# Kernel tuning notes

Measured on AMD Instinct MI355X. Metric: run time of the kernel, lower is better.

Reference implementation:

```python
import jax, jax.numpy as jnp
import numpy as np

WS = 7
NUM_HEADS = 4


def _rel_pos_index(ws):
    # Swin-style relative position index for a ws x ws window -> (ws*ws, ws*ws)
    coords = np.stack(np.meshgrid(np.arange(ws), np.arange(ws), indexing='ij'))
    flat = coords.reshape(2, -1)
    rel = (flat[:, :, None] - flat[:, None, :]).transpose(1, 2, 0)
    rel = rel + (ws - 1)
    return jnp.asarray(rel[..., 0] * (2 * ws - 1) + rel[..., 1])


def setup_inputs() -> dict:
    key = jax.random.key(0)
    ks = jax.random.split(key, 8)
    B, H, W, C = 8, 224, 224, 128
    r = C // 8  # channel-attention reduction
    s = 0.02
    return {
        'x': jax.random.normal(ks[0], (B, H * W, C), jnp.float32),
        'H': H,
        'W': W,
        'ca_w1': jax.random.normal(ks[1], (r, C), jnp.float32) * s,
        'ca_b1': jnp.zeros((r,), jnp.float32),
        'ca_w2': jax.random.normal(ks[2], (C, r), jnp.float32) * s,
        'ca_b2': jnp.zeros((C,), jnp.float32),
        'sa_w': jax.random.normal(ks[3], (1, 2, 7, 7), jnp.float32) * s,
        'sa_b': jnp.zeros((1,), jnp.float32),
        'in_proj_w': jax.random.normal(ks[4], (3 * C, C), jnp.float32) * s,
        'in_proj_b': jnp.zeros((3 * C,), jnp.float32),
        'out_proj_w': jax.random.normal(ks[5], (C, C), jnp.float32) * s,
        'out_proj_b': jnp.zeros((C,), jnp.float32),
        'rpe_table': jax.random.normal(ks[6], ((2 * WS - 1) ** 2, NUM_HEADS), jnp.float32) * s,
    }


def reference(x, H, W, ca_w1, ca_b1, ca_w2, ca_b2, sa_w, sa_b,
              in_proj_w, in_proj_b, out_proj_w, out_proj_b, rpe_table):
    B, N, C = x.shape
    x = x.reshape(B, H, W, C)

    # --- ComprehensiveAttentionalBlock (channel + spatial attention) on NCHW ---
    x4 = x.transpose(0, 3, 1, 2)  # (B, C, H, W)
    pooled = x4.mean(axis=(2, 3))  # (B, C)
    s_ca = jax.nn.sigmoid(jax.nn.relu(pooled @ ca_w1.T + ca_b1) @ ca_w2.T + ca_b2)
    x4 = x4 * s_ca[:, :, None, None]
    sa_in = jnp.concatenate([x4.mean(axis=1, keepdims=True), x4.max(axis=1, keepdims=True)], axis=1)
    sa = jax.lax.conv_general_dilated(sa_in, sa_w, (1, 1), [(3, 3), (3, 3)],
                                      dimension_numbers=('NCHW', 'OIHW', 'NCHW'))
    sa = sa + sa_b[None, :, None, None]
    x4 = x4 * jax.nn.sigmoid(sa)
    x = x4.transpose(0, 2, 3, 1)  # (B, H, W, C)

    # --- pad to multiple of window size (symmetric, as PadBlock) ---
    ph, pw = (-H) % WS, (-W) % WS
    x = jnp.pad(x, ((0, 0), (ph // 2, ph - ph // 2), (pw // 2, pw - pw // 2), (0, 0)))
    Hp, Wp = H + ph, W + pw
    nh, nw = Hp // WS, Wp // WS
    L = WS * WS
    Nb = B * nh * nw

    # --- interlaced window permute: (B,Hp,Wp,C) -> (L, Nb, C) ---
    xp = x.reshape(B, nh, WS, nw, WS, C).transpose(2, 4, 0, 1, 3, 5).reshape(L, Nb, C)

    # --- multi-head attention with relative position embedding ---
    qkv = xp @ in_proj_w.T + in_proj_b  # (L, Nb, 3C)
    q, k, v = jnp.split(qkv, 3, axis=-1)
    d = C // NUM_HEADS
    q = q.reshape(L, Nb, NUM_HEADS, d) * (d ** -0.5)
    k = k.reshape(L, Nb, NUM_HEADS, d)
    v = v.reshape(L, Nb, NUM_HEADS, d)
    scores = jnp.einsum('lnhd,mnhd->nhlm', q, k)  # (Nb, h, L, L)
    bias = rpe_table[_rel_pos_index(WS)]  # (L, L, h)
    scores = scores + bias.transpose(2, 0, 1)[None]
    attn = jax.nn.softmax(scores, axis=-1)
    out = jnp.einsum('nhlm,mnhd->lnhd', attn, v).reshape(L, Nb, C)
    out = out @ out_proj_w.T + out_proj_b

    # --- reverse permute and depad ---
    out = out.reshape(WS, WS, B, nh, nw, C).transpose(2, 3, 0, 4, 1, 5).reshape(B, Hp, Wp, C)
    out = out[:, ph // 2:ph // 2 + H, pw // 2:pw // 2 + W, :]
    return out.reshape(B, N, C)
```

## Files before the change

kernel.cpp:

```cpp
#include <hip/hip_runtime.h>

typedef unsigned short u16;
typedef __attribute__((ext_vector_type(8))) short short8;
typedef __attribute__((ext_vector_type(4))) float f32x4;
typedef __attribute__((ext_vector_type(4))) unsigned short us4;
typedef __attribute__((ext_vector_type(2))) unsigned int u32x2;

union S8U { short8 v; us4 h[2]; unsigned int u[4]; };

__device__ __forceinline__ u16 f2bf(float f){
  unsigned int u = __builtin_bit_cast(unsigned int, f);
  u += 0x7fffu + ((u >> 16) & 1u);
  return (u16)(u >> 16);
}
__device__ __forceinline__ float bf2f(u16 s){
  unsigned int u = ((unsigned int)s) << 16;
  return __builtin_bit_cast(float, u);
}
__device__ __forceinline__ unsigned int cvt2(float a, float b){
  unsigned int r;
  asm("v_cvt_pk_bf16_f32 %0, %1, %2" : "=v"(r) : "v"(a), "v"(b));
  return r;
}
#define MFMA16(a,b,c) __builtin_amdgcn_mfma_f32_16x16x32_bf16((a),(b),(c),0,0,0)

__global__ void k0_prep(const float* __restrict__ w_in, const float* __restrict__ w_out,
                        const float* __restrict__ rpe,
                        u16* __restrict__ wqkv_bf, u16* __restrict__ wout_bf,
                        u16* __restrict__ bias_bf, float* __restrict__ pooled){
  int gid = blockIdx.x * 256 + threadIdx.x;
  int stride = gridDim.x * 256;
  for (int idx = gid; idx < 83968; idx += stride) {
    if (idx < 49152) {
      wqkv_bf[idx] = f2bf(w_in[idx]);
    } else if (idx < 65536) {
      int i = idx - 49152; wout_bf[i] = f2bf(w_out[i]);
    } else if (idx < 81920) {
      int i = idx - 65536;
      int h = i >> 12, l = (i >> 6) & 63, m = i & 63;
      float v;
      if (m >= 49) v = -3.0e38f;
      else if (l >= 49) v = 0.0f;
      else {
        int il = (l * 9363) >> 16, jl = l - il * 7;
        int im = (m * 9363) >> 16, jm = m - im * 7;
        int r = (il - im + 6) * 13 + (jl - jm + 6);
        v = rpe[r * 4 + h];
      }
      bias_bf[i] = f2bf(v);
    } else {
      pooled[idx - 81920] = 0.0f;
    }
  }
}

__global__ void k1_pool(const float* __restrict__ x, float* __restrict__ pooled){
  __shared__ float4 red[4][32];
  int b = blockIdx.x / 392, s = blockIdx.x % 392;
  int t = threadIdx.x;
  int c4 = t & 31, r0 = t >> 5;
  const float4* xb = (const float4*)x + ((size_t)b * 50176 + (size_t)s * 128) * 32;
  float4 acc = {0.f, 0.f, 0.f, 0.f};
#pragma unroll
  for (int i = 0; i < 16; ++i) {
    float4 v = xb[(size_t)(r0 + 8 * i) * 32 + c4];
    acc.x += v.x; acc.y += v.y; acc.z += v.z; acc.w += v.w;
  }
  acc.x += __shfl_xor(acc.x, 32); acc.y += __shfl_xor(acc.y, 32);
  acc.z += __shfl_xor(acc.z, 32); acc.w += __shfl_xor(acc.w, 32);
  if ((t & 63) < 32) red[t >> 6][c4] = acc;
  __syncthreads();
  if (t < 32) {
    float4 a0 = red[0][t], a1 = red[1][t], a2 = red[2][t], a3 = red[3][t];
    float sx = a0.x + a1.x + a2.x + a3.x;
    float sy = a0.y + a1.y + a2.y + a3.y;
    float sz = a0.z + a1.z + a2.z + a3.z;
    float sw = a0.w + a1.w + a2.w + a3.w;
    float* p = pooled + b * 128 + t * 4;
    atomicAdd(p + 0, sx); atomicAdd(p + 1, sy);
    atomicAdd(p + 2, sz); atomicAdd(p + 3, sw);
  }
}

__global__ void k2_mlp(const float* __restrict__ pooled,
                       const float* __restrict__ w1, const float* __restrict__ b1,
                       const float* __restrict__ w2, const float* __restrict__ b2,
                       float* __restrict__ sca){
  __shared__ float hid[8][16];
  int t = threadIdx.x;
  int b = t >> 4, j = t & 15;
  float a = 0.f;
  for (int c = 0; c < 128; ++c) a += pooled[b * 128 + c] * w1[j * 128 + c];
  a = a * (1.0f / 50176.0f) + b1[j];
  hid[b][j] = fmaxf(a, 0.0f);
  __syncthreads();
  int c = t;
  for (int bb = 0; bb < 8; ++bb) {
    float v = b2[c];
    for (int jj = 0; jj < 16; ++jj) v += hid[bb][jj] * w2[c * 16 + jj];
    sca[bb * 128 + c] = 1.0f / (1.0f + __expf(-v));
  }
}

__global__ void k3_stats(const float* __restrict__ x, const float* __restrict__ sca,
                         float* __restrict__ smean, float* __restrict__ smax){
  int b = blockIdx.x / 1568, chunk = blockIdx.x % 1568;
  int t = threadIdx.x, lane = t & 63, wv = t >> 6;
  int p = lane >> 3, c8 = lane & 7;
  const float4* sc = (const float4*)(sca + b * 128 + c8 * 16);
  float4 s0 = sc[0], s1 = sc[1], s2 = sc[2], s3 = sc[3];
  int pix = chunk * 32 + wv * 8 + p;
  const float4* row = (const float4*)(x + ((size_t)b * 50176 + pix) * 128 + c8 * 16);
  float4 v0 = row[0], v1 = row[1], v2 = row[2], v3 = row[3];
  float sum = 0.f, mx = -3.0e38f;
#define ACC4(V,S) { float a0=V.x*S.x, a1=V.y*S.y, a2=V.z*S.z, a3=V.w*S.w; \
                    sum += a0+a1+a2+a3; mx = fmaxf(mx, fmaxf(fmaxf(a0,a1), fmaxf(a2,a3))); }
  ACC4(v0,s0) ACC4(v1,s1) ACC4(v2,s2) ACC4(v3,s3)
#undef ACC4
  sum += __shfl_xor(sum, 1); sum += __shfl_xor(sum, 2); sum += __shfl_xor(sum, 4);
  mx = fmaxf(mx, __shfl_xor(mx, 1));
  mx = fmaxf(mx, __shfl_xor(mx, 2));
  mx = fmaxf(mx, __shfl_xor(mx, 4));
  if (c8 == 0) {
    smean[(size_t)b * 50176 + pix] = sum * (1.0f / 128.0f);
    smax [(size_t)b * 50176 + pix] = mx;
  }
}

__global__ void k4_conv(const float* __restrict__ smean, const float* __restrict__ smax,
                        const float* __restrict__ w, const float* __restrict__ sb,
                        float* __restrict__ ssa){
  __shared__ float tM[22 * 22], tX[22 * 22], wl[98];
  int b = blockIdx.x / 196, cell = blockIdx.x % 196;
  int y0 = (cell / 14) * 16, x0 = (cell % 14) * 16;
  int t = threadIdx.x;
  if (t < 98) wl[t] = w[t];
  for (int idx = t; idx < 484; idx += 256) {
    int yy = y0 - 3 + idx / 22, xx = x0 - 3 + idx % 22;
    bool ok = (yy >= 0 && yy < 224 && xx >= 0 && xx < 224);
    tM[idx] = ok ? smean[(size_t)b * 50176 + yy * 224 + xx] : 0.0f;
    tX[idx] = ok ? smax [(size_t)b * 50176 + yy * 224 + xx] : 0.0f;
  }
  __syncthreads();
  int ty = t >> 4, tx = t & 15;
  float acc = sb[0];
  for (int ky = 0; ky < 7; ++ky)
    for (int kx = 0; kx < 7; ++kx) {
      acc += wl[ky * 7 + kx]      * tM[(ty + ky) * 22 + tx + kx];
      acc += wl[49 + ky * 7 + kx] * tX[(ty + ky) * 22 + tx + kx];
    }
  ssa[(size_t)b * 50176 + (y0 + ty) * 224 + (x0 + tx)] = 1.0f / (1.0f + __expf(-acc));
}

__global__ __launch_bounds__(256) void k5_attn(
    const float* __restrict__ x, const float* __restrict__ sca, const float* __restrict__ ssa,
    const u16* __restrict__ wqkv, const u16* __restrict__ wout, const u16* __restrict__ biasb,
    const float* __restrict__ bin, const float* __restrict__ bout, float* __restrict__ out)
{
  __shared__ u16 lds[26112];
  u16* qR = lds;
  u16* kR = lds + 8704;
  u16* vR = lds + 17408;
  float* fbuf = (float*)(lds + 8704);

  int blk = blockIdx.x;
  int b = blk >> 10, ih = (blk >> 5) & 31, iw = blk & 31;
  int t = threadIdx.x, lane = t & 63, wv = t >> 6;
  int c15 = lane & 15, g4 = lane >> 4;

  {
    int cq = t & 31, rr = t >> 5;
    const float* xb = x + (size_t)b * 50176 * 128;
    float4 s4 = *(const float4*)(sca + b * 128 + cq * 4);
    for (int p = 0; p < 7; ++p) {
      int r = p * 8 + rr;
      if (r < 49) {
        int i = (r * 9363) >> 16, j = r - i * 7;
        int hh = ih * 7 + i, ww = iw * 7 + j;
        float4 v = *(const float4*)(xb + ((size_t)(hh * 224 + ww)) * 128 + cq * 4);
        float ss = ssa[(size_t)b * 50176 + hh * 224 + ww];
        u32x2 o;
        o[0] = cvt2(v.x * s4.x * ss, v.y * s4.y * ss);
        o[1] = cvt2(v.z * s4.z * ss, v.w * s4.w * ss);
        *(u32x2*)(qR + r * 136 + cq * 4) = o;
      }
    }
    unsigned int* z = (unsigned int*)(qR + 49 * 136);
    for (int idx = t; idx < 1020; idx += 256) z[idx] = 0u;
  }
  __syncthreads();

  short8 xsf[4][4];
#pragma unroll
  for (int nt = 0; nt < 4; ++nt)
#pragma unroll
    for (int ks = 0; ks < 4; ++ks)
      xsf[nt][ks] = *(const short8*)(qR + (16 * nt + c15) * 136 + 32 * ks + 8 * g4);
  __syncthreads();

#pragma unroll
  for (int qi = 0; qi < 4; ++qi) {
    int mt = (qi < 2) ? (2 * wv + qi) : (8 + 2 * wv + qi - 2);
    short8 wf[4];
#pragma unroll
    for (int ks = 0; ks < 4; ++ks)
      wf[ks] = *(const short8*)(wqkv + (size_t)(16 * mt + c15) * 128 + 32 * ks + 8 * g4);
    float4 b4 = *(const float4*)(bin + 16 * mt + 4 * g4);
    bool isq = (qi < 2);
    float scl = isq ? 0.17677669529663689f : 1.0f;
    u16* dst = isq ? qR : kR;
    int dcol = isq ? (16 * mt) : (16 * (mt - 8));
#pragma unroll
    for (int nt = 0; nt < 4; ++nt) {
      f32x4 acc = {0.f, 0.f, 0.f, 0.f};
#pragma unroll
      for (int ks = 0; ks < 4; ++ks) acc = MFMA16(wf[ks], xsf[nt][ks], acc);
      u32x2 o;
      o[0] = cvt2((acc[0] + b4.x) * scl, (acc[1] + b4.y) * scl);
      o[1] = cvt2((acc[2] + b4.z) * scl, (acc[3] + b4.w) * scl);
      *(u32x2*)(dst + (16 * nt + c15) * 136 + dcol + 4 * g4) = o;
    }
  }
#pragma unroll
  for (int vi = 0; vi < 2; ++vi) {
    int ntv = 2 * wv + vi;
    short8 wf[4];
#pragma unroll
    for (int ks = 0; ks < 4; ++ks)
      wf[ks] = *(const short8*)(wqkv + (size_t)(256 + 16 * ntv + c15) * 128 + 32 * ks + 8 * g4);
    float bv = bin[256 + 16 * ntv + c15];
#pragma unroll
    for (int mt = 0; mt < 4; ++mt) {
      f32x4 acc = {0.f, 0.f, 0.f, 0.f};
#pragma unroll
      for (int ks = 0; ks < 4; ++ks) acc = MFMA16(xsf[mt][ks], wf[ks], acc);
      u32x2 o;
      o[0] = cvt2(acc[0] + bv, acc[1] + bv);
      o[1] = cvt2(acc[2] + bv, acc[3] + bv);
      *(u32x2*)(vR + (16 * ntv + c15) * 68 + 16 * mt + 4 * g4) = o;
    }
  }

  short8 kf[4], qf[4];
#pragma unroll
  for (int mt = 0; mt < 4; ++mt)
    kf[mt] = *(const short8*)(kR + (16 * mt + c15) * 136 + 32 * wv + 8 * g4);
#pragma unroll
  for (int nt = 0; nt < 4; ++nt)
    qf[nt] = *(const short8*)(qR + (16 * nt + c15) * 136 + 32 * wv + 8 * g4);
  f32x4 sc[4][4];
#pragma unroll
  for (int mt = 0; mt < 4; ++mt)
#pragma unroll
    for (int nt = 0; nt < 4; ++nt) {
      f32x4 zz = {0.f, 0.f, 0.f, 0.f};
      sc[mt][nt] = MFMA16(kf[mt], qf[nt], zz);
    }
#pragma unroll
  for (int mt = 0; mt < 4; ++mt)
#pragma unroll
    for (int nt = 0; nt < 4; ++nt) {
      us4 bb = *(const us4*)(biasb + (size_t)((wv * 64 + 16 * nt + c15) * 64 + 16 * mt + 4 * g4));
      sc[mt][nt][0] += bf2f(bb[0]); sc[mt][nt][1] += bf2f(bb[1]);
      sc[mt][nt][2] += bf2f(bb[2]); sc[mt][nt][3] += bf2f(bb[3]);
    }
  unsigned int pk[4][4][2];
#pragma unroll
  for (int nt = 0; nt < 4; ++nt) {
    float m = -3.0e38f;
#pragma unroll
    for (int mt = 0; mt < 4; ++mt)
      m = fmaxf(m, fmaxf(fmaxf(sc[mt][nt][0], sc[mt][nt][1]),
                         fmaxf(sc[mt][nt][2], sc[mt][nt][3])));
    m = fmaxf(m, __shfl_xor(m, 16));
    m = fmaxf(m, __shfl_xor(m, 32));
    float s = 0.f;
#pragma unroll
    for (int mt = 0; mt < 4; ++mt)
#pragma unroll
      for (int r = 0; r < 4; ++r) {
        float e = __expf(sc[mt][nt][r] - m);
        sc[mt][nt][r] = e; s += e;
      }
    s += __shfl_xor(s, 16);
    s += __shfl_xor(s, 32);
    float rs = 1.0f / s;
#pragma unroll
    for (int mt = 0; mt < 4; ++mt) {
      pk[mt][nt][0] = cvt2(sc[mt][nt][0] * rs, sc[mt][nt][1] * rs);
      pk[mt][nt][1] = cvt2(sc[mt][nt][2] * rs, sc[mt][nt][3] * rs);
    }
  }

  f32x4 oacc[2][4];
  const f32x4 zero4 = {0.f, 0.f, 0.f, 0.f};
#pragma unroll
  for (int dt = 0; dt < 2; ++dt)
#pragma unroll
    for (int nt = 0; nt < 4; ++nt) oacc[dt][nt] = zero4;
#pragma unroll
  for (int ks = 0; ks < 2; ++ks) {
    short8 va[2];
#pragma unroll
    for (int dt = 0; dt < 2; ++dt) {
      S8U u;
      u.h[0] = *(const us4*)(vR + (32 * wv + 16 * dt + c15) * 68 + 32 * ks + 4 * g4);
      u.h[1] = *(const us4*)(vR + (32 * wv + 16 * dt + c15) * 68 + 32 * ks + 16 + 4 * g4);
      va[dt] = u.v;
    }
#pragma unroll
    for (int nt = 0; nt < 4; ++nt) {
      S8U pb;
      pb.u[0] = pk[2 * ks][nt][0];     pb.u[1] = pk[2 * ks][nt][1];
      pb.u[2] = pk[2 * ks + 1][nt][0]; pb.u[3] = pk[2 * ks + 1][nt][1];
#pragma unroll
      for (int dt = 0; dt < 2; ++dt)
        oacc[dt][nt] = MFMA16(va[dt], pb.v, oacc[dt][nt]);
    }
  }
#pragma unroll
  for (int dt = 0; dt < 2; ++dt)
#pragma unroll
    for (int nt = 0; nt < 4; ++nt) {
      u32x2 o;
      o[0] = cvt2(oacc[dt][nt][0], oacc[dt][nt][1]);
      o[1] = cvt2(oacc[dt][nt][2], oacc[dt][nt][3]);
      *(u32x2*)(qR + (16 * nt + c15) * 136 + 32 * wv + 16 * dt + 4 * g4) = o;
    }
  __syncthreads();

  short8 oof[4][4];
#pragma unroll
  for (int mt = 0; mt < 4; ++mt)
#pragma unroll
    for (int ks = 0; ks < 4; ++ks)
      oof[mt][ks] = *(const short8*)(qR + (16 * mt + c15) * 136 + 32 * ks + 8 * g4);
#pragma unroll
  for (int oi = 0; oi < 2; ++oi) {
    int nto = 2 * wv + oi;
    short8 wf[4];
#pragma unroll
    for (int ks = 0; ks < 4; ++ks)
      wf[ks] = *(const short8*)(wout + (size_t)(16 * nto + c15) * 128 + 32 * ks + 8 * g4);
    float bo = bout[16 * nto + c15];
#pragma unroll
    for (int mt = 0; mt < 4; ++mt) {
      f32x4 acc = {0.f, 0.f, 0.f, 0.f};
#pragma unroll
      for (int ks = 0; ks < 4; ++ks) acc = MFMA16(oof[mt][ks], wf[ks], acc);
#pragma unroll
      for (int r = 0; r < 4; ++r)
        fbuf[(16 * mt + 4 * g4 + r) * 132 + 16 * nto + c15] = acc[r] + bo;
    }
  }
  __syncthreads();

  {
    float* ob = out + (size_t)b * 50176 * 128;
    int rr = t >> 5, c = t & 31;
#pragma unroll
    for (int it = 0; it < 7; ++it) {
      int tok = it * 8 + rr;
      if (tok < 49) {
        int i = (tok * 9363) >> 16, j = tok - i * 7;
        int hh = ih * 7 + i, ww = iw * 7 + j;
        float4 vv = *(const float4*)(fbuf + tok * 132 + c * 4);
        *(float4*)(ob + ((size_t)(hh * 224 + ww)) * 128 + c * 4) = vv;
      }
    }
  }
}

extern "C" void kernel_launch(void* const* d_in, const int* in_sizes, int n_in,
                              void* d_out, int out_size, void* d_ws, size_t ws_size,
                              hipStream_t stream) {
  const float* x     = (const float*)d_in[0];
  const float* ca_w1 = (const float*)d_in[3];
  const float* ca_b1 = (const float*)d_in[4];
  const float* ca_w2 = (const float*)d_in[5];
  const float* ca_b2 = (const float*)d_in[6];
  const float* sa_w  = (const float*)d_in[7];
  const float* sa_b  = (const float*)d_in[8];
  const float* w_in  = (const float*)d_in[9];
  const float* b_in  = (const float*)d_in[10];
  const float* w_out = (const float*)d_in[11];
  const float* b_out = (const float*)d_in[12];
  const float* rpe   = (const float*)d_in[13];
  float* out = (float*)d_out;

  char* ws = (char*)d_ws;
  float* pooled = (float*)(ws + 0);
  float* sca    = (float*)(ws + 4096);
  float* smean  = (float*)(ws + 8192);
  float* smax   = (float*)(ws + 8192 + 1605632);
  float* ssa    = (float*)(ws + 8192 + 2 * 1605632);
  u16* wqkv_bf  = (u16*)(ws + 8192 + 3 * 1605632);
  u16* wout_bf  = (u16*)(ws + 8192 + 3 * 1605632 + 98304);
  u16* bias_bf  = (u16*)(ws + 8192 + 3 * 1605632 + 98304 + 32768);

  k0_prep<<<328, 256, 0, stream>>>(w_in, w_out, rpe, wqkv_bf, wout_bf, bias_bf, pooled);
  k1_pool<<<3136, 256, 0, stream>>>(x, pooled);
  k2_mlp <<<1, 128, 0, stream>>>(pooled, ca_w1, ca_b1, ca_w2, ca_b2, sca);
  k3_stats<<<12544, 256, 0, stream>>>(x, sca, smean, smax);
  k4_conv<<<1568, 256, 0, stream>>>(smean, smax, sa_w, sa_b, ssa);
  k5_attn<<<8192, 256, 0, stream>>>(x, sca, ssa, wqkv_bf, wout_bf, bias_bf, b_in, b_out, out);
}
```

Baseline: 659.7 us.

## Shrink attention LDS by aliasing K and V buffers; fold fp32 bias into MFMA accumulator

The attention kernel's shared memory drops from three bf16 tiles to two. K fragments are read into registers before the V tile overwrites the same region, and the output staging buffer reuses the Q region after an extra barrier. The relative-position bias is now stored as fp32 and loaded directly as the MFMA accumulator init, which removes the separate bf16 unpack-and-add pass. The intent is higher occupancy from lower LDS use, paid for with extra __syncthreads and a larger bias table read.

Measured after the change: 671.2 us. Within noise of the previous version (+1.7%).

```diff
diff --git a/kernel.cpp b/kernel.cpp
--- a/kernel.cpp
+++ b/kernel.cpp
@@ -13,10 +13,6 @@
   u += 0x7fffu + ((u >> 16) & 1u);
   return (u16)(u >> 16);
 }
-__device__ __forceinline__ float bf2f(u16 s){
-  unsigned int u = ((unsigned int)s) << 16;
-  return __builtin_bit_cast(float, u);
-}
 __device__ __forceinline__ unsigned int cvt2(float a, float b){
   unsigned int r;
   asm("v_cvt_pk_bf16_f32 %0, %1, %2" : "=v"(r) : "v"(a), "v"(b));
@@ -27,7 +23,7 @@
 __global__ void k0_prep(const float* __restrict__ w_in, const float* __restrict__ w_out,
                         const float* __restrict__ rpe,
                         u16* __restrict__ wqkv_bf, u16* __restrict__ wout_bf,
-                        u16* __restrict__ bias_bf, float* __restrict__ pooled){
+                        float* __restrict__ biasf, float* __restrict__ pooled){
   int gid = blockIdx.x * 256 + threadIdx.x;
   int stride = gridDim.x * 256;
   for (int idx = gid; idx < 83968; idx += stride) {
@@ -47,7 +43,7 @@
         int r = (il - im + 6) * 13 + (jl - jm + 6);
         v = rpe[r * 4 + h];
       }
-      bias_bf[i] = f2bf(v);
+      biasf[i] = v;
     } else {
       pooled[idx - 81920] = 0.0f;
     }
@@ -154,14 +150,13 @@
 
 __global__ __launch_bounds__(256) void k5_attn(
     const float* __restrict__ x, const float* __restrict__ sca, const float* __restrict__ ssa,
-    const u16* __restrict__ wqkv, const u16* __restrict__ wout, const u16* __restrict__ biasb,
+    const u16* __restrict__ wqkv, const u16* __restrict__ wout, const float* __restrict__ biasf,
     const float* __restrict__ bin, const float* __restrict__ bout, float* __restrict__ out)
 {
-  __shared__ u16 lds[26112];
-  u16* qR = lds;
-  u16* kR = lds + 8704;
-  u16* vR = lds + 17408;
-  float* fbuf = (float*)(lds + 8704);
+  __shared__ u16 lds[17408];
+  u16* qR  = lds;
+  u16* kvR = lds + 8704;
+  float* fbuf = (float*)lds;
 
   int blk = blockIdx.x;
   int b = blk >> 10, ih = (blk >> 5) & 31, iw = blk & 31;
@@ -208,7 +203,7 @@
     float4 b4 = *(const float4*)(bin + 16 * mt + 4 * g4);
     bool isq = (qi < 2);
     float scl = isq ? 0.17677669529663689f : 1.0f;
-    u16* dst = isq ? qR : kR;
+    u16* dst = isq ? qR : kvR;
     int dcol = isq ? (16 * mt) : (16 * (mt - 8));
 #pragma unroll
     for (int nt = 0; nt < 4; ++nt) {
@@ -221,6 +216,16 @@
       *(u32x2*)(dst + (16 * nt + c15) * 136 + dcol + 4 * g4) = o;
     }
   }
+
+  short8 kf[4], qf[4];
+#pragma unroll
+  for (int mt = 0; mt < 4; ++mt)
+    kf[mt] = *(const short8*)(kvR + (16 * mt + c15) * 136 + 32 * wv + 8 * g4);
+#pragma unroll
+  for (int nt = 0; nt < 4; ++nt)
+    qf[nt] = *(const short8*)(qR + (16 * nt + c15) * 136 + 32 * wv + 8 * g4);
+  __syncthreads();
+
 #pragma unroll
   for (int vi = 0; vi < 2; ++vi) {
     int ntv = 2 * wv + vi;
@@ -237,32 +242,17 @@
       u32x2 o;
       o[0] = cvt2(acc[0] + bv, acc[1] + bv);
       o[1] = cvt2(acc[2] + bv, acc[3] + bv);
-      *(u32x2*)(vR + (16 * ntv + c15) * 68 + 16 * mt + 4 * g4) = o;
-    }
-  }
-
-  short8 kf[4], qf[4];
+      *(u32x2*)(kvR + (16 * ntv + c15) * 68 + 16 * mt + 4 * g4) = o;
+    }
+  }
+
+  f32x4 sc[4][4];
 #pragma unroll
   for (int mt = 0; mt < 4; ++mt)
-    kf[mt] = *(const short8*)(kR + (16 * mt + c15) * 136 + 32 * wv + 8 * g4);
-#pragma unroll
-  for (int nt = 0; nt < 4; ++nt)
-    qf[nt] = *(const short8*)(qR + (16 * nt + c15) * 136 + 32 * wv + 8 * g4);
-  f32x4 sc[4][4];
-#pragma unroll
-  for (int mt = 0; mt < 4; ++mt)
 #pragma unroll
     for (int nt = 0; nt < 4; ++nt) {
-      f32x4 zz = {0.f, 0.f, 0.f, 0.f};
-      sc[mt][nt] = MFMA16(kf[mt], qf[nt], zz);
-    }
-#pragma unroll
-  for (int mt = 0; mt < 4; ++mt)
-#pragma unroll
-    for (int nt = 0; nt < 4; ++nt) {
-      us4 bb = *(const us4*)(biasb + (size_t)((wv * 64 + 16 * nt + c15) * 64 + 16 * mt + 4 * g4));
-      sc[mt][nt][0] += bf2f(bb[0]); sc[mt][nt][1] += bf2f(bb[1]);
-      sc[mt][nt][2] += bf2f(bb[2]); sc[mt][nt][3] += bf2f(bb[3]);
+      f32x4 bc = *(const f32x4*)(biasf + (size_t)(wv * 64 + 16 * nt + c15) * 64 + 16 * mt + 4 * g4);
+      sc[mt][nt] = MFMA16(kf[mt], qf[nt], bc);
     }
   unsigned int pk[4][4][2];
 #pragma unroll
@@ -304,8 +294,8 @@
 #pragma unroll
     for (int dt = 0; dt < 2; ++dt) {
       S8U u;
-      u.h[0] = *(const us4*)(vR + (32 * wv + 16 * dt + c15) * 68 + 32 * ks + 4 * g4);
-      u.h[1] = *(const us4*)(vR + (32 * wv + 16 * dt + c15) * 68 + 32 * ks + 16 + 4 * g4);
+      u.h[0] = *(const us4*)(kvR + (32 * wv + 16 * dt + c15) * 68 + 32 * ks + 4 * g4);
+      u.h[1] = *(const us4*)(kvR + (32 * wv + 16 * dt + c15) * 68 + 32 * ks + 16 + 4 * g4);
       va[dt] = u.v;
     }
 #pragma unroll
@@ -335,6 +325,8 @@
 #pragma unroll
     for (int ks = 0; ks < 4; ++ks)
       oof[mt][ks] = *(const short8*)(qR + (16 * mt + c15) * 136 + 32 * ks + 8 * g4);
+  __syncthreads();
+
 #pragma unroll
   for (int oi = 0; oi < 2; ++oi) {
     int nto = 2 * wv + oi;
@@ -396,12 +388,12 @@
   float* ssa    = (float*)(ws + 8192 + 2 * 1605632);
   u16* wqkv_bf  = (u16*)(ws + 8192 + 3 * 1605632);
   u16* wout_bf  = (u16*)(ws + 8192 + 3 * 1605632 + 98304);
-  u16* bias_bf  = (u16*)(ws + 8192 + 3 * 1605632 + 98304 + 32768);
-
-  k0_prep<<<328, 256, 0, stream>>>(w_in, w_out, rpe, wqkv_bf, wout_bf, bias_bf, pooled);
+  float* biasf  = (float*)(ws + 8192 + 3 * 1605632 + 98304 + 32768);
+
+  k0_prep<<<328, 256, 0, stream>>>(w_in, w_out, rpe, wqkv_bf, wout_bf, biasf, pooled);
   k1_pool<<<3136, 256, 0, stream>>>(x, pooled);
   k2_mlp <<<1, 128, 0, stream>>>(pooled, ca_w1, ca_b1, ca_w2, ca_b2, sca);
   k3_stats<<<12544, 256, 0, stream>>>(x, sca, smean, smax);
   k4_conv<<<1568, 256, 0, stream>>>(smean, smax, sa_w, sa_b, ssa);
-  k5_attn<<<8192, 256, 0, stream>>>(x, sca, ssa, wqkv_bf, wout_bf, bias_bf, b_in, b_out, out);
-}
+  k5_attn<<<8192, 256, 0, stream>>>(x, sca, ssa, wqkv_bf, wout_bf, biasf, b_in, b_out, out);
+}
```
